# Optimization experiments

Measured on AMD Instinct MI355X. Metric: run time of the kernel, lower is better.

Reference implementation:

```python
import jax, jax.numpy as jnp
import numpy as np
from jax import lax

THR = 0.0
NMS_SIZE = 5
PAD = NMS_SIZE // 2
B, C, H, W = 8, 1, 2048, 2048
# Upper bound on number of surviving peaks: ~1/(2*25) of pixels pass in
# expectation for iid noise; B*H*W//8 is a very safe static cap.
MAX_PEAKS = (B * H * W) // 8


def max_filter(x):
    # torch MaxPool2d(kernel=5, stride=1, padding=2) == max reduce_window
    # with -inf padding, same spatial output shape.
    return lax.reduce_window(
        x, -jnp.inf, lax.max,
        window_dimensions=(1, 1, NMS_SIZE, NMS_SIZE),
        window_strides=(1, 1, 1, 1),
        padding=[(0, 0), (0, 0), (PAD, PAD), (PAD, PAD)],
    )


def setup_inputs() -> dict:
    key = jax.random.key(0)
    scores = jax.random.normal(key, (B, C, H, W), dtype=jnp.float32)
    return {"scores": scores}


def reference(scores):
    # maxima = (scores == maxpool(scores)) & (scores > thr)
    maxima = (scores == max_filter(scores)) & (scores > THR)
    # torch: maxima.nonzero().t()[2:4] -> [2, K] rows = (h, w) coords.
    # jit-safe: fixed-size nonzero, padded with -1 for absent entries.
    idx = jnp.nonzero(maxima, size=MAX_PEAKS, fill_value=-1)
    return jnp.stack([idx[2], idx[3]])  # [2, MAX_PEAKS]
```

## Files before the change

kernel.cpp:

```cpp
#include <hip/hip_runtime.h>
#include <math.h>

#define IMG_W 2048
#define IMG_H 2048
#define BATCH 8
#define MAX_PEAKS ((BATCH * IMG_H * IMG_W) / 8)
#define NWORDS (BATCH * IMG_H * IMG_W / 32)
#define ROWSW 32
#define NFILL 2048

__global__ __launch_bounds__(256, 4) void nms_mask(const float* __restrict__ scores,
                                                   unsigned* __restrict__ words,
                                                   unsigned* __restrict__ bsum2) {
    const int t = threadIdx.x;
    const int lane = t & 63;
    const int wv = t >> 6;
    const int b = blockIdx.x;
    const int img = b >> 7;
    const int rem = b & 127;
    const int strip = rem >> 4;
    const int chunk = rem & 15;
    const int r0 = chunk * 128 + wv * ROWSW;
    const int c0 = strip * 256;
    const int cl = c0 + lane * 4;
    const size_t imgBase = (size_t)img * (IMG_H * IMG_W);

    const float* colp = scores + imgBase + cl;
    const bool leftHalf = (lane < 32);
    const bool isL = (lane == 0), isR = (lane == 63);
    const int ecol = leftHalf ? (c0 - 4) : (c0 + 256);
    const bool evalid = ((unsigned)ecol < IMG_W);
    const int ecolC = evalid ? ecol : c0;
    const float* ecolp2 = scores + imgBase + ecolC + (leftHalf ? 2 : 0);

    const float NEG = -INFINITY;
    float4 R[12];
    float2 E[12];

#pragma unroll
    for (int m = 0; m < 11; ++m) {
        int gr = r0 - 2 + m;
        int rc = gr < 0 ? 0 : gr;
        size_t off = (size_t)rc * IMG_W;
        R[m] = *(const float4*)(colp + off);
        E[m] = *(const float2*)(ecolp2 + off);
    }
    if (r0 == 0) {
#pragma unroll
        for (int m = 0; m < 2; ++m) {
            R[m] = make_float4(NEG, NEG, NEG, NEG);
            E[m] = make_float2(NEG, NEG);
        }
    }
    const bool bot = (r0 + 32) >= IMG_H;

    unsigned cnt = 0;
    const int shamt = (lane & 7) * 4;
    size_t wIdx = (size_t)(img * IMG_H + r0) * (IMG_W / 32) + strip * 8 + (lane >> 3);
    const int cb0 = (img * IMG_H + r0) >> 4;
    const bool writer = ((lane & 7) == 0);

#pragma unroll
    for (int i = 0; i < 32; ++i) {
        if (i < 25) {
            int gr = r0 + 9 + i;
            int rc = gr > IMG_H - 1 ? IMG_H - 1 : gr;
            size_t off = (size_t)rc * IMG_W;
            float4 v = *(const float4*)(colp + off);
            float2 e = *(const float2*)(ecolp2 + off);
            if (i >= 23) {
                if (bot) {
                    v = make_float4(NEG, NEG, NEG, NEG);
                    e = make_float2(NEG, NEG);
                }
            }
            R[(11 + i) % 12] = v;
            E[(11 + i) % 12] = e;
        }

        const float4 w0 = R[(i) % 12];
        const float4 w1 = R[(i + 1) % 12];
        const float4 mid = R[(i + 2) % 12];
        const float4 w3 = R[(i + 3) % 12];
        const float4 w4 = R[(i + 4) % 12];
        float vmx = fmaxf(fmaxf(fmaxf(w0.x, w1.x), fmaxf(mid.x, w3.x)), w4.x);
        float vmy = fmaxf(fmaxf(fmaxf(w0.y, w1.y), fmaxf(mid.y, w3.y)), w4.y);
        float vmz = fmaxf(fmaxf(fmaxf(w0.z, w1.z), fmaxf(mid.z, w3.z)), w4.z);
        float vmw = fmaxf(fmaxf(fmaxf(w0.w, w1.w), fmaxf(mid.w, w3.w)), w4.w);
        const float2 e0 = E[(i) % 12];
        const float2 e1 = E[(i + 1) % 12];
        const float2 e2 = E[(i + 2) % 12];
        const float2 e3 = E[(i + 3) % 12];
        const float2 e4 = E[(i + 4) % 12];
        float vex = fmaxf(fmaxf(fmaxf(e0.x, e1.x), fmaxf(e2.x, e3.x)), e4.x);
        float vey = fmaxf(fmaxf(fmaxf(e0.y, e1.y), fmaxf(e2.y, e3.y)), e4.y);
        float eX = evalid ? vex : NEG;
        float eY = evalid ? vey : NEG;

        float A = __shfl_up(vmz, 1);
        float B = __shfl_up(vmw, 1);
        float C = __shfl_down(vmx, 1);
        float D = __shfl_down(vmy, 1);
        if (isL) { A = eX; B = eY; }
        if (isR) { C = eX; D = eY; }

        float t12 = fmaxf(vmy, vmz);
        float m02 = fmaxf(vmx, t12);
        float m03 = fmaxf(m02, vmw);
        float m13 = fmaxf(t12, vmw);
        float h0 = fmaxf(fmaxf(A, B), m02);
        float h1 = fmaxf(B, m03);
        float h2 = fmaxf(m03, C);
        float h3 = fmaxf(m13, fmaxf(C, D));

        unsigned nib = 0;
        nib |= (mid.x > 0.0f && mid.x >= h0) ? 1u : 0u;
        nib |= (mid.y > 0.0f && mid.y >= h1) ? 2u : 0u;
        nib |= (mid.z > 0.0f && mid.z >= h2) ? 4u : 0u;
        nib |= (mid.w > 0.0f && mid.w >= h3) ? 8u : 0u;

        unsigned wd = nib << shamt;
        wd |= __shfl_xor(wd, 1);
        wd |= __shfl_xor(wd, 2);
        wd |= __shfl_xor(wd, 4);
        if (writer) {
            words[wIdx] = wd;
            cnt += __popc(wd);
        }
        wIdx += IMG_W / 32;

        if (i == 15 || i == 31) {
            unsigned s = cnt;
            s += __shfl_xor(s, 1);
            s += __shfl_xor(s, 2);
            s += __shfl_xor(s, 4);
            s += __shfl_xor(s, 8);
            s += __shfl_xor(s, 16);
            s += __shfl_xor(s, 32);
            if (lane == 0) bsum2[(cb0 + (i >> 4)) * 8 + strip] = s;
            cnt = 0;
        }
    }
}

__global__ __launch_bounds__(256) void nms_scan(const unsigned* __restrict__ bsum2,
                                                unsigned* __restrict__ base) {
    __shared__ unsigned wtot[4];
    const int t = threadIdx.x;
    const int lane = t & 63, wid = t >> 6;
    const uint4* p = (const uint4*)(bsum2 + t * 32);
    unsigned c[4];
#pragma unroll
    for (int i = 0; i < 4; ++i) {
        uint4 a = p[2 * i], bq = p[2 * i + 1];
        c[i] = a.x + a.y + a.z + a.w + bq.x + bq.y + bq.z + bq.w;
    }
    unsigned s0 = c[0], s1 = s0 + c[1], s2 = s1 + c[2], ts = s2 + c[3];
    unsigned sc = ts;
#pragma unroll
    for (int d = 1; d < 64; d <<= 1) {
        unsigned o = __shfl_up(sc, d);
        if (lane >= d) sc += o;
    }
    if (lane == 63) wtot[wid] = sc;
    __syncthreads();
    unsigned wpre = 0;
#pragma unroll
    for (int k = 0; k < 4; ++k) wpre += (k < wid) ? wtot[k] : 0u;
    unsigned excl = wpre + sc - ts;
    ((uint4*)base)[t] = make_uint4(excl, excl + s0, excl + s1, excl + s2);
    if (t == 255) base[1024] = wpre + sc;
}

__global__ __launch_bounds__(256) void nms_compact(const unsigned* __restrict__ words,
                                                   const unsigned* __restrict__ base,
                                                   int* __restrict__ out) {
    const int t = threadIdx.x;
    const int b = blockIdx.x;
    if (b < 1024) {
        __shared__ unsigned wq[4];
        const int lane = t & 63, wid = t >> 6;
        uint4 q = ((const uint4*)(words + b * 1024))[t];
        unsigned wv[4] = {q.x, q.y, q.z, q.w};
        unsigned tsum = __popc(wv[0]) + __popc(wv[1]) + __popc(wv[2]) + __popc(wv[3]);
        unsigned sc = tsum;
#pragma unroll
        for (int d = 1; d < 64; d <<= 1) {
            unsigned o = __shfl_up(sc, d);
            if (lane >= d) sc += o;
        }
        if (lane == 63) wq[wid] = sc;
        __syncthreads();
        unsigned wpre = 0;
#pragma unroll
        for (int k = 0; k < 4; ++k) wpre += (k < wid) ? wq[k] : 0u;
        unsigned off = base[b] + wpre + sc - tsum;

        const unsigned gword0 = (unsigned)b * 1024u + (unsigned)t * 4u;
#pragma unroll
        for (int wi = 0; wi < 4; ++wi) {
            unsigned m = wv[wi];
            unsigned pbase = (gword0 + wi) << 5;
            while (m) {
                int bit = __builtin_ctz(m);
                m &= m - 1;
                unsigned ppix = pbase + (unsigned)bit;
                int hh = (int)((ppix >> 11) & 2047u);
                int ww = (int)(ppix & 2047u);
                if (off < (unsigned)MAX_PEAKS) {
                    out[off] = hh;
                    out[MAX_PEAKS + off] = ww;
                }
                ++off;
            }
        }
    } else {
        unsigned total = base[1024];
        if (total > (unsigned)MAX_PEAKS) total = MAX_PEAKS;
        unsigned tail = (unsigned)MAX_PEAKS - total;
        unsigned fb = (unsigned)(b - 1024);
        unsigned per = (tail + NFILL - 1) / NFILL;
        unsigned s = total + fb * per;
        unsigned e = s + per;
        if (e > (unsigned)MAX_PEAKS) e = MAX_PEAKS;
        for (unsigned k = s + t; k < e; k += 256) {
            out[k] = -1;
            out[MAX_PEAKS + k] = -1;
        }
    }
}

extern "C" void kernel_launch(void* const* d_in, const int* in_sizes, int n_in,
                              void* d_out, int out_size, void* d_ws, size_t ws_size,
                              hipStream_t stream) {
    const float* scores = (const float*)d_in[0];
    int* out = (int*)d_out;
    unsigned* words = (unsigned*)d_ws;
    unsigned* bsum2 = words + NWORDS;
    unsigned* base = bsum2 + 8192;

    nms_mask<<<1024, 256, 0, stream>>>(scores, words, bsum2);
    nms_scan<<<1, 256, 0, stream>>>(bsum2, base);
    nms_compact<<<1024 + NFILL, 256, 0, stream>>>(words, base, out);
}
```

Measured before the change: 215.1 us.

## Fuse scan into compact kernel via atomic election and halve mask rows per wave

The separate single-block scan kernel is removed. The first block of the finish kernel to win an atomicCAS computes the block prefix sums and publishes a release flag, and all other blocks spin-wait on that flag before compacting. The mask kernel now gives each wave 16 rows instead of 32, doubles the grid and raises the occupancy hint, which shrinks the register ring buffer. This saves one kernel launch gap, at the cost of a spin-wait whose forward progress depends on the winner block being scheduled, and of more halo reloads per row.

```diff
diff --git a/kernel.cpp b/kernel.cpp
--- a/kernel.cpp
+++ b/kernel.cpp
@@ -6,21 +6,22 @@
 #define BATCH 8
 #define MAX_PEAKS ((BATCH * IMG_H * IMG_W) / 8)
 #define NWORDS (BATCH * IMG_H * IMG_W / 32)
-#define ROWSW 32
 #define NFILL 2048
 
-__global__ __launch_bounds__(256, 4) void nms_mask(const float* __restrict__ scores,
+__global__ __launch_bounds__(256, 5) void nms_mask(const float* __restrict__ scores,
                                                    unsigned* __restrict__ words,
-                                                   unsigned* __restrict__ bsum2) {
+                                                   unsigned* __restrict__ bsum2,
+                                                   unsigned* __restrict__ ctrl) {
+    if (blockIdx.x == 0 && threadIdx.x == 0) { ctrl[0] = 0u; ctrl[1] = 0u; }
     const int t = threadIdx.x;
     const int lane = t & 63;
     const int wv = t >> 6;
     const int b = blockIdx.x;
-    const int img = b >> 7;
-    const int rem = b & 127;
-    const int strip = rem >> 4;
-    const int chunk = rem & 15;
-    const int r0 = chunk * 128 + wv * ROWSW;
+    const int img = b >> 8;
+    const int rem = b & 255;
+    const int strip = rem >> 5;
+    const int chunk = rem & 31;
+    const int r0 = chunk * 64 + wv * 16;
     const int c0 = strip * 256;
     const int cl = c0 + lane * 4;
     const size_t imgBase = (size_t)img * (IMG_H * IMG_W);
@@ -34,11 +35,11 @@
     const float* ecolp2 = scores + imgBase + ecolC + (leftHalf ? 2 : 0);
 
     const float NEG = -INFINITY;
-    float4 R[12];
-    float2 E[12];
-
-#pragma unroll
-    for (int m = 0; m < 11; ++m) {
+    float4 R[8];
+    float2 E[8];
+
+#pragma unroll
+    for (int m = 0; m < 7; ++m) {
         int gr = r0 - 2 + m;
         int rc = gr < 0 ? 0 : gr;
         size_t off = (size_t)rc * IMG_W;
@@ -46,52 +47,47 @@
         E[m] = *(const float2*)(ecolp2 + off);
     }
     if (r0 == 0) {
-#pragma unroll
-        for (int m = 0; m < 2; ++m) {
-            R[m] = make_float4(NEG, NEG, NEG, NEG);
-            E[m] = make_float2(NEG, NEG);
-        }
-    }
-    const bool bot = (r0 + 32) >= IMG_H;
+        R[0] = R[1] = make_float4(NEG, NEG, NEG, NEG);
+        E[0] = E[1] = make_float2(NEG, NEG);
+    }
+    const bool bot = (r0 + 16) >= IMG_H;
 
     unsigned cnt = 0;
     const int shamt = (lane & 7) * 4;
     size_t wIdx = (size_t)(img * IMG_H + r0) * (IMG_W / 32) + strip * 8 + (lane >> 3);
-    const int cb0 = (img * IMG_H + r0) >> 4;
+    const int cb = (img * IMG_H + r0) >> 4;
     const bool writer = ((lane & 7) == 0);
 
 #pragma unroll
-    for (int i = 0; i < 32; ++i) {
-        if (i < 25) {
-            int gr = r0 + 9 + i;
+    for (int i = 0; i < 16; ++i) {
+        if (i < 13) {
+            int gr = r0 + 5 + i;
             int rc = gr > IMG_H - 1 ? IMG_H - 1 : gr;
             size_t off = (size_t)rc * IMG_W;
             float4 v = *(const float4*)(colp + off);
             float2 e = *(const float2*)(ecolp2 + off);
-            if (i >= 23) {
-                if (bot) {
-                    v = make_float4(NEG, NEG, NEG, NEG);
-                    e = make_float2(NEG, NEG);
-                }
+            if (i >= 11 && bot) {
+                v = make_float4(NEG, NEG, NEG, NEG);
+                e = make_float2(NEG, NEG);
             }
-            R[(11 + i) % 12] = v;
-            E[(11 + i) % 12] = e;
-        }
-
-        const float4 w0 = R[(i) % 12];
-        const float4 w1 = R[(i + 1) % 12];
-        const float4 mid = R[(i + 2) % 12];
-        const float4 w3 = R[(i + 3) % 12];
-        const float4 w4 = R[(i + 4) % 12];
+            R[(7 + i) & 7] = v;
+            E[(7 + i) & 7] = e;
+        }
+
+        const float4 w0 = R[(i) & 7];
+        const float4 w1 = R[(i + 1) & 7];
+        const float4 mid = R[(i + 2) & 7];
+        const float4 w3 = R[(i + 3) & 7];
+        const float4 w4 = R[(i + 4) & 7];
         float vmx = fmaxf(fmaxf(fmaxf(w0.x, w1.x), fmaxf(mid.x, w3.x)), w4.x);
         float vmy = fmaxf(fmaxf(fmaxf(w0.y, w1.y), fmaxf(mid.y, w3.y)), w4.y);
         float vmz = fmaxf(fmaxf(fmaxf(w0.z, w1.z), fmaxf(mid.z, w3.z)), w4.z);
         float vmw = fmaxf(fmaxf(fmaxf(w0.w, w1.w), fmaxf(mid.w, w3.w)), w4.w);
-        const float2 e0 = E[(i) % 12];
-        const float2 e1 = E[(i + 1) % 12];
-        const float2 e2 = E[(i + 2) % 12];
-        const float2 e3 = E[(i + 3) % 12];
-        const float2 e4 = E[(i + 4) % 12];
+        const float2 e0 = E[(i) & 7];
+        const float2 e1 = E[(i + 1) & 7];
+        const float2 e2 = E[(i + 2) & 7];
+        const float2 e3 = E[(i + 3) & 7];
+        const float2 e4 = E[(i + 4) & 7];
         float vex = fmaxf(fmaxf(fmaxf(e0.x, e1.x), fmaxf(e2.x, e3.x)), e4.x);
         float vey = fmaxf(fmaxf(fmaxf(e0.y, e1.y), fmaxf(e2.y, e3.y)), e4.y);
         float eX = evalid ? vex : NEG;
@@ -128,59 +124,74 @@
             cnt += __popc(wd);
         }
         wIdx += IMG_W / 32;
-
-        if (i == 15 || i == 31) {
-            unsigned s = cnt;
-            s += __shfl_xor(s, 1);
-            s += __shfl_xor(s, 2);
-            s += __shfl_xor(s, 4);
-            s += __shfl_xor(s, 8);
-            s += __shfl_xor(s, 16);
-            s += __shfl_xor(s, 32);
-            if (lane == 0) bsum2[(cb0 + (i >> 4)) * 8 + strip] = s;
-            cnt = 0;
-        }
-    }
+    }
+
+    unsigned s = cnt;
+    s += __shfl_xor(s, 1);
+    s += __shfl_xor(s, 2);
+    s += __shfl_xor(s, 4);
+    s += __shfl_xor(s, 8);
+    s += __shfl_xor(s, 16);
+    s += __shfl_xor(s, 32);
+    if (lane == 0) bsum2[cb * 8 + strip] = s;
 }
 
-__global__ __launch_bounds__(256) void nms_scan(const unsigned* __restrict__ bsum2,
-                                                unsigned* __restrict__ base) {
-    __shared__ unsigned wtot[4];
-    const int t = threadIdx.x;
-    const int lane = t & 63, wid = t >> 6;
-    const uint4* p = (const uint4*)(bsum2 + t * 32);
-    unsigned c[4];
-#pragma unroll
-    for (int i = 0; i < 4; ++i) {
-        uint4 a = p[2 * i], bq = p[2 * i + 1];
-        c[i] = a.x + a.y + a.z + a.w + bq.x + bq.y + bq.z + bq.w;
-    }
-    unsigned s0 = c[0], s1 = s0 + c[1], s2 = s1 + c[2], ts = s2 + c[3];
-    unsigned sc = ts;
-#pragma unroll
-    for (int d = 1; d < 64; d <<= 1) {
-        unsigned o = __shfl_up(sc, d);
-        if (lane >= d) sc += o;
-    }
-    if (lane == 63) wtot[wid] = sc;
-    __syncthreads();
-    unsigned wpre = 0;
-#pragma unroll
-    for (int k = 0; k < 4; ++k) wpre += (k < wid) ? wtot[k] : 0u;
-    unsigned excl = wpre + sc - ts;
-    ((uint4*)base)[t] = make_uint4(excl, excl + s0, excl + s1, excl + s2);
-    if (t == 255) base[1024] = wpre + sc;
-}
-
-__global__ __launch_bounds__(256) void nms_compact(const unsigned* __restrict__ words,
-                                                   const unsigned* __restrict__ base,
-                                                   int* __restrict__ out) {
+__global__ __launch_bounds__(256) void nms_finish(const unsigned* __restrict__ words,
+                                                  const unsigned* __restrict__ bsum2,
+                                                  unsigned* __restrict__ base,
+                                                  unsigned* __restrict__ ctrl,
+                                                  int* __restrict__ out) {
     const int t = threadIdx.x;
     const int b = blockIdx.x;
+    const int lane = t & 63, wid = t >> 6;
+
+    uint4 q = make_uint4(0u, 0u, 0u, 0u);
+    if (b < 1024) q = ((const uint4*)(words + b * 1024))[t];
+
+    __shared__ unsigned sWin;
+    if (t == 0) {
+        unsigned old = atomicCAS(&ctrl[0], 0u, (unsigned)b + 1u);
+        sWin = (old == 0u) ? 1u : 0u;
+    }
+    __syncthreads();
+
+    if (sWin) {
+        __shared__ unsigned wtot[4];
+        const uint4* p = (const uint4*)(bsum2 + t * 32);
+        unsigned c[4];
+#pragma unroll
+        for (int i = 0; i < 4; ++i) {
+            uint4 a = p[2 * i], bq = p[2 * i + 1];
+            c[i] = a.x + a.y + a.z + a.w + bq.x + bq.y + bq.z + bq.w;
+        }
+        unsigned s0 = c[0], s1 = s0 + c[1], s2 = s1 + c[2], ts = s2 + c[3];
+        unsigned sc = ts;
+#pragma unroll
+        for (int d = 1; d < 64; d <<= 1) {
+            unsigned o = __shfl_up(sc, d);
+            if (lane >= d) sc += o;
+        }
+        if (lane == 63) wtot[wid] = sc;
+        __syncthreads();
+        unsigned wpre = 0;
+#pragma unroll
+        for (int k = 0; k < 4; ++k) wpre += (k < wid) ? wtot[k] : 0u;
+        unsigned excl = wpre + sc - ts;
+        ((uint4*)base)[t] = make_uint4(excl, excl + s0, excl + s1, excl + s2);
+        if (t == 255) base[1024] = wpre + sc;
+        __threadfence();
+        __syncthreads();
+        if (t == 0)
+            __hip_atomic_store(&ctrl[1], 1u, __ATOMIC_RELEASE,
+                               __HIP_MEMORY_SCOPE_AGENT);
+    }
+
+    while (__hip_atomic_load(&ctrl[1], __ATOMIC_ACQUIRE,
+                             __HIP_MEMORY_SCOPE_AGENT) != 1u)
+        __builtin_amdgcn_s_sleep(32);
+
     if (b < 1024) {
         __shared__ unsigned wq[4];
-        const int lane = t & 63, wid = t >> 6;
-        uint4 q = ((const uint4*)(words + b * 1024))[t];
         unsigned wv[4] = {q.x, q.y, q.z, q.w};
         unsigned tsum = __popc(wv[0]) + __popc(wv[1]) + __popc(wv[2]) + __popc(wv[3]);
         unsigned sc = tsum;
@@ -238,8 +249,8 @@
     unsigned* words = (unsigned*)d_ws;
     unsigned* bsum2 = words + NWORDS;
     unsigned* base = bsum2 + 8192;
-
-    nms_mask<<<1024, 256, 0, stream>>>(scores, words, bsum2);
-    nms_scan<<<1, 256, 0, stream>>>(bsum2, base);
-    nms_compact<<<1024 + NFILL, 256, 0, stream>>>(words, base, out);
+    unsigned* ctrl = base + 1028;
+
+    nms_mask<<<2048, 256, 0, stream>>>(scores, words, bsum2, ctrl);
+    nms_finish<<<1024 + NFILL, 256, 0, stream>>>(words, bsum2, base, ctrl, out);
 }
```

Result: slower. 503.5 us (+134.1%).

## Load overlapping left/right float4 windows per lane instead of shuffling halos

Applied to the files above, without the earlier changes.

Each lane now loads two overlapping float4s (columns cl-2..cl+1 and cl+2..cl+5), with clamping at the image edges, instead of one float4 plus a float2 edge-column load and cross-lane shuffles for the horizontal halo. This removes the four shuffles per row and the per-wave halo handling, and shrinks the register ring from 12 to 8 rows. In exchange it issues twice the float4 global loads, relying on cache hits for the overlap, and does vertical max on 8 columns instead of 6. The popcount is also moved to every lane on its own nibble instead of only the writer lanes.

```diff
diff --git a/kernel.cpp b/kernel.cpp
--- a/kernel.cpp
+++ b/kernel.cpp
@@ -6,7 +6,6 @@
 #define BATCH 8
 #define MAX_PEAKS ((BATCH * IMG_H * IMG_W) / 8)
 #define NWORDS (BATCH * IMG_H * IMG_W / 32)
-#define ROWSW 32
 #define NFILL 2048
 
 __global__ __launch_bounds__(256, 4) void nms_mask(const float* __restrict__ scores,
@@ -20,37 +19,30 @@
     const int rem = b & 127;
     const int strip = rem >> 4;
     const int chunk = rem & 15;
-    const int r0 = chunk * 128 + wv * ROWSW;
+    const int r0 = chunk * 128 + wv * 32;
     const int c0 = strip * 256;
     const int cl = c0 + lane * 4;
     const size_t imgBase = (size_t)img * (IMG_H * IMG_W);
 
-    const float* colp = scores + imgBase + cl;
-    const bool leftHalf = (lane < 32);
-    const bool isL = (lane == 0), isR = (lane == 63);
-    const int ecol = leftHalf ? (c0 - 4) : (c0 + 256);
-    const bool evalid = ((unsigned)ecol < IMG_W);
-    const int ecolC = evalid ? ecol : c0;
-    const float* ecolp2 = scores + imgBase + ecolC + (leftHalf ? 2 : 0);
+    const bool lclamp = (cl == 0);
+    const bool rclamp = (cl == IMG_W - 4);
+    const float* Lp = scores + imgBase + (lclamp ? 0 : cl - 2);
+    const float* Rp = scores + imgBase + (rclamp ? (IMG_W - 4) : cl + 2);
 
     const float NEG = -INFINITY;
-    float4 R[12];
-    float2 E[12];
-
-#pragma unroll
-    for (int m = 0; m < 11; ++m) {
+    float4 RL[8], RR[8];
+
+#pragma unroll
+    for (int m = 0; m < 7; ++m) {
         int gr = r0 - 2 + m;
         int rc = gr < 0 ? 0 : gr;
         size_t off = (size_t)rc * IMG_W;
-        R[m] = *(const float4*)(colp + off);
-        E[m] = *(const float2*)(ecolp2 + off);
+        RL[m] = *(const float4*)(Lp + off);
+        RR[m] = *(const float4*)(Rp + off);
     }
     if (r0 == 0) {
-#pragma unroll
-        for (int m = 0; m < 2; ++m) {
-            R[m] = make_float4(NEG, NEG, NEG, NEG);
-            E[m] = make_float2(NEG, NEG);
-        }
+        RL[0] = RL[1] = make_float4(NEG, NEG, NEG, NEG);
+        RR[0] = RR[1] = make_float4(NEG, NEG, NEG, NEG);
     }
     const bool bot = (r0 + 32) >= IMG_H;
 
@@ -62,71 +54,69 @@
 
 #pragma unroll
     for (int i = 0; i < 32; ++i) {
-        if (i < 25) {
-            int gr = r0 + 9 + i;
+        if (i < 29) {
+            int gr = r0 + 5 + i;
             int rc = gr > IMG_H - 1 ? IMG_H - 1 : gr;
             size_t off = (size_t)rc * IMG_W;
-            float4 v = *(const float4*)(colp + off);
-            float2 e = *(const float2*)(ecolp2 + off);
-            if (i >= 23) {
-                if (bot) {
-                    v = make_float4(NEG, NEG, NEG, NEG);
-                    e = make_float2(NEG, NEG);
-                }
+            float4 lv = *(const float4*)(Lp + off);
+            float4 rv = *(const float4*)(Rp + off);
+            if (i >= 27 && bot) {
+                lv = make_float4(NEG, NEG, NEG, NEG);
+                rv = make_float4(NEG, NEG, NEG, NEG);
             }
-            R[(11 + i) % 12] = v;
-            E[(11 + i) % 12] = e;
-        }
-
-        const float4 w0 = R[(i) % 12];
-        const float4 w1 = R[(i + 1) % 12];
-        const float4 mid = R[(i + 2) % 12];
-        const float4 w3 = R[(i + 3) % 12];
-        const float4 w4 = R[(i + 4) % 12];
-        float vmx = fmaxf(fmaxf(fmaxf(w0.x, w1.x), fmaxf(mid.x, w3.x)), w4.x);
-        float vmy = fmaxf(fmaxf(fmaxf(w0.y, w1.y), fmaxf(mid.y, w3.y)), w4.y);
-        float vmz = fmaxf(fmaxf(fmaxf(w0.z, w1.z), fmaxf(mid.z, w3.z)), w4.z);
-        float vmw = fmaxf(fmaxf(fmaxf(w0.w, w1.w), fmaxf(mid.w, w3.w)), w4.w);
-        const float2 e0 = E[(i) % 12];
-        const float2 e1 = E[(i + 1) % 12];
-        const float2 e2 = E[(i + 2) % 12];
-        const float2 e3 = E[(i + 3) % 12];
-        const float2 e4 = E[(i + 4) % 12];
-        float vex = fmaxf(fmaxf(fmaxf(e0.x, e1.x), fmaxf(e2.x, e3.x)), e4.x);
-        float vey = fmaxf(fmaxf(fmaxf(e0.y, e1.y), fmaxf(e2.y, e3.y)), e4.y);
-        float eX = evalid ? vex : NEG;
-        float eY = evalid ? vey : NEG;
-
-        float A = __shfl_up(vmz, 1);
-        float B = __shfl_up(vmw, 1);
-        float C = __shfl_down(vmx, 1);
-        float D = __shfl_down(vmy, 1);
-        if (isL) { A = eX; B = eY; }
-        if (isR) { C = eX; D = eY; }
-
-        float t12 = fmaxf(vmy, vmz);
-        float m02 = fmaxf(vmx, t12);
-        float m03 = fmaxf(m02, vmw);
-        float m13 = fmaxf(t12, vmw);
-        float h0 = fmaxf(fmaxf(A, B), m02);
-        float h1 = fmaxf(B, m03);
-        float h2 = fmaxf(m03, C);
-        float h3 = fmaxf(m13, fmaxf(C, D));
+            RL[(7 + i) & 7] = lv;
+            RR[(7 + i) & 7] = rv;
+        }
+
+        const float4 a0 = RL[(i) & 7],     b0 = RR[(i) & 7];
+        const float4 a1 = RL[(i + 1) & 7], b1 = RR[(i + 1) & 7];
+        const float4 a2 = RL[(i + 2) & 7], b2 = RR[(i + 2) & 7];
+        const float4 a3 = RL[(i + 3) & 7], b3 = RR[(i + 3) & 7];
+        const float4 a4 = RL[(i + 4) & 7], b4 = RR[(i + 4) & 7];
+        float Lvx = fmaxf(fmaxf(fmaxf(a0.x, a1.x), fmaxf(a2.x, a3.x)), a4.x);
+        float Lvy = fmaxf(fmaxf(fmaxf(a0.y, a1.y), fmaxf(a2.y, a3.y)), a4.y);
+        float Lvz = fmaxf(fmaxf(fmaxf(a0.z, a1.z), fmaxf(a2.z, a3.z)), a4.z);
+        float Lvw = fmaxf(fmaxf(fmaxf(a0.w, a1.w), fmaxf(a2.w, a3.w)), a4.w);
+        float Rvx = fmaxf(fmaxf(fmaxf(b0.x, b1.x), fmaxf(b2.x, b3.x)), b4.x);
+        float Rvy = fmaxf(fmaxf(fmaxf(b0.y, b1.y), fmaxf(b2.y, b3.y)), b4.y);
+        float Rvz = fmaxf(fmaxf(fmaxf(b0.z, b1.z), fmaxf(b2.z, b3.z)), b4.z);
+        float Rvw = fmaxf(fmaxf(fmaxf(b0.w, b1.w), fmaxf(b2.w, b3.w)), b4.w);
+
+        float v0 = lclamp ? NEG : Lvx;
+        float v1 = lclamp ? NEG : Lvy;
+        float v2 = lclamp ? Lvx : Lvz;
+        float v3 = lclamp ? Lvy : Lvw;
+        float v4 = rclamp ? Rvz : Rvx;
+        float v5 = rclamp ? Rvw : Rvy;
+        float v6 = rclamp ? NEG : Rvz;
+        float v7 = rclamp ? NEG : Rvw;
+
+        float m12 = fmaxf(v1, v2);
+        float m34 = fmaxf(v3, v4);
+        float m56 = fmaxf(v5, v6);
+        float h0 = fmaxf(fmaxf(v0, m12), m34);
+        float h1 = fmaxf(fmaxf(m12, m34), v5);
+        float h2 = fmaxf(fmaxf(v2, m34), m56);
+        float h3 = fmaxf(fmaxf(m34, m56), v7);
+
+        const float4 Lm = a2, Rm = b2;
+        float s0 = lclamp ? Lm.x : Lm.z;
+        float s1 = lclamp ? Lm.y : Lm.w;
+        float s2 = rclamp ? Rm.z : Rm.x;
+        float s3 = rclamp ? Rm.w : Rm.y;
 
         unsigned nib = 0;
-        nib |= (mid.x > 0.0f && mid.x >= h0) ? 1u : 0u;
-        nib |= (mid.y > 0.0f && mid.y >= h1) ? 2u : 0u;
-        nib |= (mid.z > 0.0f && mid.z >= h2) ? 4u : 0u;
-        nib |= (mid.w > 0.0f && mid.w >= h3) ? 8u : 0u;
+        nib |= (s0 > 0.0f && s0 >= h0) ? 1u : 0u;
+        nib |= (s1 > 0.0f && s1 >= h1) ? 2u : 0u;
+        nib |= (s2 > 0.0f && s2 >= h2) ? 4u : 0u;
+        nib |= (s3 > 0.0f && s3 >= h3) ? 8u : 0u;
+        cnt += __popc(nib);
 
         unsigned wd = nib << shamt;
         wd |= __shfl_xor(wd, 1);
         wd |= __shfl_xor(wd, 2);
         wd |= __shfl_xor(wd, 4);
-        if (writer) {
-            words[wIdx] = wd;
-            cnt += __popc(wd);
-        }
+        if (writer) words[wIdx] = wd;
         wIdx += IMG_W / 32;
 
         if (i == 15 || i == 31) {
```

Measured after the change: 213.9 us. Within noise of the previous version (-0.6%).
